# Kernel optimization log

Measured on AMD Instinct MI355X. Metric: run time of the kernel, lower is better.

The kernel has to match this reference:

```python
import jax, jax.numpy as jnp
import numpy as np

N_NODES = 50000
N_EDGES = 640000
N_REL = 8
IN_DIM = 128
HID_DIM = 128
OUT_DIM = 64


def setup_inputs() -> dict:
    key = jax.random.key(0)
    ks = jax.random.split(key, 8)
    features = jax.random.normal(ks[0], (N_NODES, IN_DIM), dtype=jnp.float32)
    src = jax.random.randint(ks[1], (N_EDGES,), 0, N_NODES, dtype=jnp.int32)
    dst = jax.random.randint(ks[2], (N_EDGES,), 0, N_NODES, dtype=jnp.int32)
    edge_types = jax.random.randint(ks[3], (N_EDGES,), 0, N_REL, dtype=jnp.int32)
    s1 = 1.0 / np.sqrt(IN_DIM)
    s2 = 1.0 / np.sqrt(HID_DIM)
    W1 = jax.random.normal(ks[4], (N_REL, IN_DIM, HID_DIM), dtype=jnp.float32) * s1
    W1_self = jax.random.normal(ks[5], (IN_DIM, HID_DIM), dtype=jnp.float32) * s1
    b1 = jnp.zeros((HID_DIM,), dtype=jnp.float32)
    W2 = jax.random.normal(ks[6], (N_REL, HID_DIM, OUT_DIM), dtype=jnp.float32) * s2
    W2_self = jax.random.normal(ks[7], (HID_DIM, OUT_DIM), dtype=jnp.float32) * s2
    b2 = jnp.zeros((OUT_DIM,), dtype=jnp.float32)
    return {"features": features, "src": src, "dst": dst, "edge_types": edge_types,
            "W1": W1, "W1_self": W1_self, "b1": b1,
            "W2": W2, "W2_self": W2_self, "b2": b2}


def _rel_graph_conv(h, src, dst, edge_types, W, W_self, b):
    # Precompute relation-specific transforms for all nodes: [R, N, Dout]
    rel = jnp.einsum('nd,rdo->rno', h, W)
    # Gather per-edge message W[etype(e)] @ h[src(e)]: [E, Dout]
    msg = rel[edge_types, src]
    # Scatter-sum to destination nodes
    agg = jax.ops.segment_sum(msg, dst, num_segments=h.shape[0])
    # Self-loop + bias (DGL RelGraphConv defaults: self_loop=True, bias=True)
    return agg + h @ W_self + b


def reference(features, src, dst, edge_types, W1, W1_self, b1, W2, W2_self, b2):
    h = jax.nn.relu(_rel_graph_conv(features, src, dst, edge_types, W1, W1_self, b1))
    logits = _rel_graph_conv(h, src, dst, edge_types, W2, W2_self, b2)
    return logits
```

## Files before the change

### kernel.cpp

```cpp
#include <hip/hip_runtime.h>
#include <hip/hip_bf16.h>
#include <stdint.h>

#define NN 50000
#define NE 640000
#define NR 8
#define NK (NR * NN)
#define NB2 ((NK + 1023) / 1024)

typedef short bf16x8 __attribute__((ext_vector_type(8)));
typedef float f32x4  __attribute__((ext_vector_type(4)));

__device__ __forceinline__ unsigned short f2bf(float f) {
    union { float f; unsigned u; } v; v.f = f;
    unsigned r = v.u + 0x7FFF + ((v.u >> 16) & 1);
    return (unsigned short)(r >> 16);
}

__global__ __launch_bounds__(256) void prep_all(
        const int* __restrict__ dst, const int* __restrict__ et, int* __restrict__ counts,
        const float* __restrict__ X, unsigned short* __restrict__ Xbf,
        const float* __restrict__ W1, const float* __restrict__ W1s, unsigned short* __restrict__ W1T,
        const float* __restrict__ W2, const float* __restrict__ W2s, unsigned short* __restrict__ W2T) {
    int b = blockIdx.x, t = threadIdx.x;
    if (b < 2500) {
        int e = b * 256 + t;
        atomicAdd(&counts[et[e] * NN + dst[e]], 1);
    } else if (b < 5625) {
        int i = (b - 2500) * 256 + t;
        const float4* pp = (const float4*)X + (size_t)i * 2;
        float4 a = pp[0], c = pp[1];
        uint4 o;
        o.x = (unsigned)f2bf(a.x) | ((unsigned)f2bf(a.y) << 16);
        o.y = (unsigned)f2bf(a.z) | ((unsigned)f2bf(a.w) << 16);
        o.z = (unsigned)f2bf(c.x) | ((unsigned)f2bf(c.y) << 16);
        o.w = (unsigned)f2bf(c.z) | ((unsigned)f2bf(c.w) << 16);
        ((uint4*)Xbf)[i] = o;
    } else if (b < 6201) {
        int idx = (b - 5625) * 256 + t;
        int k = idx & 127, c = idx >> 7;
        int r = c >> 7, o = c & 127;
        float v = (r < 8) ? W1[((size_t)r * 128 + k) * 128 + o]
                          : W1s[(size_t)k * 128 + o];
        W1T[idx] = f2bf(v);
    } else {
        int idx = (b - 6201) * 256 + t;
        int k = idx & 127, c = idx >> 7;
        int r = c / 64, o = c - r * 64;
        float v = (r < 8) ? W2[((size_t)r * 128 + k) * 64 + o]
                          : W2s[(size_t)k * 64 + o];
        W2T[idx] = f2bf(v);
    }
}

__global__ __launch_bounds__(1024) void blocksum_kernel(const int* __restrict__ counts,
                                                        int* __restrict__ bsum, int n) {
    __shared__ int ws[16];
    int i = blockIdx.x * 1024 + threadIdx.x;
    int v = (i < n) ? counts[i] : 0;
    #pragma unroll
    for (int d = 32; d > 0; d >>= 1) v += __shfl_down(v, d, 64);
    int wid = threadIdx.x >> 6, lane = threadIdx.x & 63;
    if (lane == 0) ws[wid] = v;
    __syncthreads();
    if (threadIdx.x < 16) {
        int s = ws[threadIdx.x];
        #pragma unroll
        for (int d = 8; d > 0; d >>= 1) s += __shfl_down(s, d, 16);
        if (threadIdx.x == 0) bsum[blockIdx.x] = s;
    }
}

__global__ __launch_bounds__(512) void scanbase_kernel(const int* __restrict__ bsum,
                                                       int* __restrict__ base,
                                                       int* __restrict__ total, int nb) {
    __shared__ int ws[8];
    int t = threadIdx.x, lane = t & 63, wid = t >> 6;
    int v = (t < nb) ? bsum[t] : 0;
    int incl = v;
    #pragma unroll
    for (int d = 1; d < 64; d <<= 1) {
        int nv = __shfl_up(incl, d, 64);
        if (lane >= d) incl += nv;
    }
    if (lane == 63) ws[wid] = incl;
    __syncthreads();
    if (t < 8) {
        int s = ws[t], si = s;
        #pragma unroll
        for (int d = 1; d < 8; d <<= 1) {
            int nv = __shfl_up(si, d, 64);
            if (t >= d) si += nv;
        }
        ws[t] = si - s;
    }
    __syncthreads();
    int excl = ws[wid] + incl - v;
    if (t < nb) base[t] = excl;
    if (t == 511) total[0] = ws[7] + incl;
}

__global__ __launch_bounds__(1024) void scanlocal_kernel(const int* __restrict__ counts,
                                                         const int* __restrict__ base,
                                                         int* __restrict__ offsets,
                                                         int* __restrict__ cursor, int n) {
    __shared__ int ws[16];
    __shared__ int wbase[16];
    int t = threadIdx.x;
    int i = blockIdx.x * 1024 + t;
    int v = (i < n) ? counts[i] : 0;
    int lane = t & 63, wid = t >> 6;
    int incl = v;
    #pragma unroll
    for (int d = 1; d < 64; d <<= 1) {
        int nv = __shfl_up(incl, d, 64);
        if (lane >= d) incl += nv;
    }
    if (lane == 63) ws[wid] = incl;
    __syncthreads();
    if (t < 16) {
        int s = ws[t], si = s;
        #pragma unroll
        for (int d = 1; d < 16; d <<= 1) {
            int nv = __shfl_up(si, d, 16);
            if (t >= d) si += nv;
        }
        wbase[t] = si - s;
    }
    __syncthreads();
    if (i < n) {
        int excl = base[blockIdx.x] + wbase[wid] + incl - v;
        offsets[i] = excl;
        cursor[i]  = excl;
    }
}

__global__ void fill2_kernel(const int* __restrict__ src, const int* __restrict__ dst,
                             const int* __restrict__ et, int* __restrict__ cursor,
                             int* __restrict__ esrc) {
    int e = blockIdx.x * 256 + threadIdx.x;
    if (e < NE) {
        int pos = atomicAdd(&cursor[et[e] * NN + dst[e]], 1);
        esrc[pos] = src[e];
    }
}

template<int NOUT, bool RELU, bool OUTBF16>
__global__ __launch_bounds__(256) void fused_layer(
        const unsigned short* __restrict__ A,
        const unsigned short* __restrict__ WT,
        const float* __restrict__ bias,
        const int* __restrict__ off2,
        const int* __restrict__ esrc,
        void* __restrict__ outp, int M) {
    constexpr int CW = NOUT / 4;
    constexpr int NJ = CW / 16;
    __shared__ unsigned short Asw[64 * 128];

    const int t = threadIdx.x;
    const int n0 = blockIdx.x * 64;
    const int bm = (M - n0 < 64) ? (M - n0) : 64;
    const int lane = t & 63;
    const int w = t >> 6;
    const int r15 = lane & 15;
    const int q = lane >> 4;

    const int key = t >> 2;
    const int sub = t & 3;
    const int kk = n0 + key;
    const bool kv = (kk < M);

    f32x4 acc[4][NJ] = {};

    auto do_mfma = [&](int rr) {
        #pragma unroll
        for (int ks = 0; ks < 4; ks++) {
            int c = (ks * 4 + q) ^ r15;
            bf16x8 af[4];
            #pragma unroll
            for (int i = 0; i < 4; i++)
                af[i] = *(const bf16x8*)((const char*)Asw + (i * 16 + r15) * 256 + (c << 4));
            #pragma unroll
            for (int j = 0; j < NJ; j++) {
                bf16x8 bf = *(const bf16x8*)(WT +
                    ((size_t)(rr * NOUT + w * CW + j * 16 + r15) << 7) + ks * 32 + q * 8);
                #pragma unroll
                for (int i = 0; i < 4; i++)
                    acc[i][j] = __builtin_amdgcn_mfma_f32_16x16x32_bf16(af[i], bf, acc[i][j], 0, 0, 0);
            }
        }
    };

    int e0 = kv ? off2[kk] : 0;
    int e1 = kv ? off2[kk + 1] : 0;

    #pragma unroll
    for (int kc = 0; kc < 4; kc++) {
        int g = t + kc * 256;
        int row = g >> 4, c = g & 15;
        uint4 v = make_uint4(0, 0, 0, 0);
        if (row < bm) v = *(const uint4*)(A + ((size_t)(n0 + row) << 7) + c * 8);
        *(uint4*)((char*)Asw + row * 256 + ((c ^ (row & 15)) << 4)) = v;
    }
    __syncthreads();
    do_mfma(8);

    for (int r = 0; r < 8; r++) {
        int e0n = 0, e1n = 0;
        if (r < 7 && kv) {
            e0n = off2[(r + 1) * NN + kk];
            e1n = off2[(r + 1) * NN + kk + 1];
        }

        float a[32];
        #pragma unroll
        for (int i = 0; i < 32; i++) a[i] = 0.f;

        const unsigned* base = (const unsigned*)A;
        for (int e = e0; e < e1; e += 4) {
            int rem = e1 - e;
            int i1 = (rem > 1) ? 1 : 0, i2 = (rem > 2) ? 2 : 0, i3 = (rem > 3) ? 3 : 0;
            int ss[4];
            ss[0] = esrc[e];
            ss[1] = esrc[e + i1];
            ss[2] = esrc[e + i2];
            ss[3] = esrc[e + i3];
            float wts[4];
            wts[0] = 1.f;
            wts[1] = i1 ? 1.f : 0.f;
            wts[2] = i2 ? 1.f : 0.f;
            wts[3] = i3 ? 1.f : 0.f;
            uint4 va[4][4];
            #pragma unroll
            for (int i = 0; i < 4; i++) {
                const uint4* rp = (const uint4*)(base + ((size_t)ss[i] << 6) + sub * 16);
                #pragma unroll
                for (int u = 0; u < 4; u++) va[i][u] = rp[u];
            }
            #pragma unroll
            for (int i = 0; i < 4; i++) {
                #pragma unroll
                for (int u = 0; u < 4; u++) {
                    unsigned uu[4] = {va[i][u].x, va[i][u].y, va[i][u].z, va[i][u].w};
                    #pragma unroll
                    for (int j = 0; j < 4; j++) {
                        a[u * 8 + j * 2 + 0] = fmaf(wts[i], __uint_as_float(uu[j] << 16), a[u * 8 + j * 2 + 0]);
                        a[u * 8 + j * 2 + 1] = fmaf(wts[i], __uint_as_float(uu[j] & 0xffff0000u), a[u * 8 + j * 2 + 1]);
                    }
                }
            }
        }
        __syncthreads();

        #pragma unroll
        for (int c4 = 0; c4 < 4; ++c4) {
            uint4 pv;
            pv.x = (unsigned)f2bf(a[c4 * 8 + 0]) | ((unsigned)f2bf(a[c4 * 8 + 1]) << 16);
            pv.y = (unsigned)f2bf(a[c4 * 8 + 2]) | ((unsigned)f2bf(a[c4 * 8 + 3]) << 16);
            pv.z = (unsigned)f2bf(a[c4 * 8 + 4]) | ((unsigned)f2bf(a[c4 * 8 + 5]) << 16);
            pv.w = (unsigned)f2bf(a[c4 * 8 + 6]) | ((unsigned)f2bf(a[c4 * 8 + 7]) << 16);
            int c = sub * 4 + c4;
            *(uint4*)((char*)Asw + key * 256 + ((c ^ (key & 15)) << 4)) = pv;
        }
        __syncthreads();

        do_mfma(r);
        e0 = e0n; e1 = e1n;
    }

    #pragma unroll
    for (int j = 0; j < NJ; j++) {
        int col = w * CW + j * 16 + r15;
        float bv = bias[col];
        #pragma unroll
        for (int i = 0; i < 4; i++) {
            #pragma unroll
            for (int reg = 0; reg < 4; reg++) {
                int m = n0 + i * 16 + q * 4 + reg;
                if (m < M) {
                    float v = acc[i][j][reg] + bv;
                    if (RELU) v = fmaxf(v, 0.f);
                    if (OUTBF16)
                        ((unsigned short*)outp)[(size_t)m * NOUT + col] = f2bf(v);
                    else
                        ((float*)outp)[(size_t)m * NOUT + col] = v;
                }
            }
        }
    }
}

extern "C" void kernel_launch(void* const* d_in, const int* in_sizes, int n_in,
                              void* d_out, int out_size, void* d_ws, size_t ws_size,
                              hipStream_t stream) {
    const float* X   = (const float*)d_in[0];
    const int*   src = (const int*)d_in[1];
    const int*   dst = (const int*)d_in[2];
    const int*   et  = (const int*)d_in[3];
    const float* W1  = (const float*)d_in[4];
    const float* W1s = (const float*)d_in[5];
    const float* b1  = (const float*)d_in[6];
    const float* W2  = (const float*)d_in[7];
    const float* W2s = (const float*)d_in[8];
    const float* b2  = (const float*)d_in[9];
    float* out = (float*)d_out;

    char* p = (char*)d_ws;
    unsigned short* Xbf = (unsigned short*)p; p += (size_t)NN * 128 * 2;
    unsigned short* hbf = (unsigned short*)p; p += (size_t)NN * 128 * 2;
    unsigned short* W1T = (unsigned short*)p; p += (size_t)9 * 128 * 128 * 2;
    unsigned short* W2T = (unsigned short*)p; p += (size_t)9 * 64 * 128 * 2;
    int* counts2 = (int*)p; p += (size_t)NK * 4;
    int* off2    = (int*)p; p += (size_t)(NK + 4) * 4;
    int* cursor2 = (int*)p; p += (size_t)NK * 4;
    int* esrc    = (int*)p; p += (size_t)NE * 4;
    int* bsum    = (int*)p; p += 512 * 4;
    int* bbase   = (int*)p; p += 512 * 4;

    hipMemsetAsync(counts2, 0, (size_t)NK * sizeof(int), stream);
    prep_all<<<6489, 256, 0, stream>>>(dst, et, counts2, X, Xbf,
                                       W1, W1s, W1T, W2, W2s, W2T);

    blocksum_kernel<<<NB2, 1024, 0, stream>>>(counts2, bsum, NK);
    scanbase_kernel<<<1, 512, 0, stream>>>(bsum, bbase, &off2[NK], NB2);
    scanlocal_kernel<<<NB2, 1024, 0, stream>>>(counts2, bbase, off2, cursor2, NK);
    fill2_kernel<<<(NE + 255) / 256, 256, 0, stream>>>(src, dst, et, cursor2, esrc);

    const int nblk = (NN + 63) / 64;

    fused_layer<128, true, true><<<nblk, 256, 0, stream>>>(
        Xbf, W1T, b1, off2, esrc, hbf, NN);
    fused_layer<64, false, false><<<nblk, 256, 0, stream>>>(
        hbf, W2T, b2, off2, esrc, out, NN);
}
```

Measured before the change: 327.9 us.

## Process two relations per iteration with double LDS buffers in fused layer

```diff
diff --git a/kernel.cpp b/kernel.cpp
--- a/kernel.cpp
+++ b/kernel.cpp
@@ -155,7 +155,7 @@
         void* __restrict__ outp, int M) {
     constexpr int CW = NOUT / 4;
     constexpr int NJ = CW / 16;
-    __shared__ unsigned short Asw[64 * 128];
+    __shared__ unsigned short Asw[2][64 * 128];
 
     const int t = threadIdx.x;
     const int n0 = blockIdx.x * 64;
@@ -172,14 +172,14 @@
 
     f32x4 acc[4][NJ] = {};
 
-    auto do_mfma = [&](int rr) {
+    auto do_mfma = [&](int b, int rr) {
         #pragma unroll
         for (int ks = 0; ks < 4; ks++) {
             int c = (ks * 4 + q) ^ r15;
             bf16x8 af[4];
             #pragma unroll
             for (int i = 0; i < 4; i++)
-                af[i] = *(const bf16x8*)((const char*)Asw + (i * 16 + r15) * 256 + (c << 4));
+                af[i] = *(const bf16x8*)((const char*)Asw[b] + (i * 16 + r15) * 256 + (c << 4));
             #pragma unroll
             for (int j = 0; j < NJ; j++) {
                 bf16x8 bf = *(const bf16x8*)(WT +
@@ -191,8 +191,24 @@
         }
     };
 
-    int e0 = kv ? off2[kk] : 0;
-    int e1 = kv ? off2[kk + 1] : 0;
+    auto accum32 = [&](float* a, const uint4* v, float wt) {
+        #pragma unroll
+        for (int u = 0; u < 4; u++) {
+            unsigned uu[4] = {v[u].x, v[u].y, v[u].z, v[u].w};
+            #pragma unroll
+            for (int j = 0; j < 4; j++) {
+                a[u * 8 + j * 2 + 0] = fmaf(wt, __uint_as_float(uu[j] << 16), a[u * 8 + j * 2 + 0]);
+                a[u * 8 + j * 2 + 1] = fmaf(wt, __uint_as_float(uu[j] & 0xffff0000u), a[u * 8 + j * 2 + 1]);
+            }
+        }
+    };
+
+    const unsigned* base = (const unsigned*)A;
+
+    int eA0 = kv ? off2[kk] : 0;
+    int eA1 = kv ? off2[kk + 1] : 0;
+    int eB0 = kv ? off2[NN + kk] : 0;
+    int eB1 = kv ? off2[NN + kk + 1] : 0;
 
     #pragma unroll
     for (int kc = 0; kc < 4; kc++) {
@@ -200,72 +216,98 @@
         int row = g >> 4, c = g & 15;
         uint4 v = make_uint4(0, 0, 0, 0);
         if (row < bm) v = *(const uint4*)(A + ((size_t)(n0 + row) << 7) + c * 8);
-        *(uint4*)((char*)Asw + row * 256 + ((c ^ (row & 15)) << 4)) = v;
-    }
-    __syncthreads();
-    do_mfma(8);
-
-    for (int r = 0; r < 8; r++) {
-        int e0n = 0, e1n = 0;
-        if (r < 7 && kv) {
-            e0n = off2[(r + 1) * NN + kk];
-            e1n = off2[(r + 1) * NN + kk + 1];
-        }
-
-        float a[32];
-        #pragma unroll
-        for (int i = 0; i < 32; i++) a[i] = 0.f;
-
-        const unsigned* base = (const unsigned*)A;
-        for (int e = e0; e < e1; e += 4) {
-            int rem = e1 - e;
-            int i1 = (rem > 1) ? 1 : 0, i2 = (rem > 2) ? 2 : 0, i3 = (rem > 3) ? 3 : 0;
-            int ss[4];
-            ss[0] = esrc[e];
-            ss[1] = esrc[e + i1];
-            ss[2] = esrc[e + i2];
-            ss[3] = esrc[e + i3];
-            float wts[4];
-            wts[0] = 1.f;
-            wts[1] = i1 ? 1.f : 0.f;
-            wts[2] = i2 ? 1.f : 0.f;
-            wts[3] = i3 ? 1.f : 0.f;
-            uint4 va[4][4];
-            #pragma unroll
-            for (int i = 0; i < 4; i++) {
-                const uint4* rp = (const uint4*)(base + ((size_t)ss[i] << 6) + sub * 16);
-                #pragma unroll
-                for (int u = 0; u < 4; u++) va[i][u] = rp[u];
-            }
-            #pragma unroll
-            for (int i = 0; i < 4; i++) {
-                #pragma unroll
-                for (int u = 0; u < 4; u++) {
-                    unsigned uu[4] = {va[i][u].x, va[i][u].y, va[i][u].z, va[i][u].w};
-                    #pragma unroll
-                    for (int j = 0; j < 4; j++) {
-                        a[u * 8 + j * 2 + 0] = fmaf(wts[i], __uint_as_float(uu[j] << 16), a[u * 8 + j * 2 + 0]);
-                        a[u * 8 + j * 2 + 1] = fmaf(wts[i], __uint_as_float(uu[j] & 0xffff0000u), a[u * 8 + j * 2 + 1]);
-                    }
-                }
-            }
+        *(uint4*)((char*)Asw[0] + row * 256 + ((c ^ (row & 15)) << 4)) = v;
+    }
+    __syncthreads();
+    do_mfma(0, 8);
+
+    #pragma unroll 1
+    for (int p = 0; p < 4; p++) {
+        const int rA = 2 * p, rB = 2 * p + 1;
+        int nA0 = 0, nA1 = 0, nB0 = 0, nB1 = 0;
+        if (p < 3 && kv) {
+            nA0 = off2[(rA + 2) * NN + kk];
+            nA1 = off2[(rA + 2) * NN + kk + 1];
+            nB0 = off2[(rB + 2) * NN + kk];
+            nB1 = off2[(rB + 2) * NN + kk + 1];
+        }
+
+        float a0[32], a1[32];
+        #pragma unroll
+        for (int i = 0; i < 32; i++) { a0[i] = 0.f; a1[i] = 0.f; }
+
+        int eA = eA0, eB = eB0;
+        while (eA < eA1 && eB < eB1) {
+            int av = (eA + 1 < eA1) ? 1 : 0;
+            int bv = (eB + 1 < eB1) ? 1 : 0;
+            int sA0 = esrc[eA], sA1 = esrc[eA + av];
+            int sB0 = esrc[eB], sB1 = esrc[eB + bv];
+            const uint4* pA0 = (const uint4*)(base + ((size_t)sA0 << 6) + sub * 16);
+            const uint4* pA1 = (const uint4*)(base + ((size_t)sA1 << 6) + sub * 16);
+            const uint4* pB0 = (const uint4*)(base + ((size_t)sB0 << 6) + sub * 16);
+            const uint4* pB1 = (const uint4*)(base + ((size_t)sB1 << 6) + sub * 16);
+            uint4 vA0[4], vA1[4], vB0[4], vB1[4];
+            #pragma unroll
+            for (int u = 0; u < 4; u++) vA0[u] = pA0[u];
+            #pragma unroll
+            for (int u = 0; u < 4; u++) vA1[u] = pA1[u];
+            #pragma unroll
+            for (int u = 0; u < 4; u++) vB0[u] = pB0[u];
+            #pragma unroll
+            for (int u = 0; u < 4; u++) vB1[u] = pB1[u];
+            accum32(a0, vA0, 1.f); accum32(a0, vA1, av ? 1.f : 0.f);
+            accum32(a1, vB0, 1.f); accum32(a1, vB1, bv ? 1.f : 0.f);
+            eA += 2; eB += 2;
+        }
+        while (eA < eA1) {
+            int av = (eA + 1 < eA1) ? 1 : 0;
+            int sA0 = esrc[eA], sA1 = esrc[eA + av];
+            const uint4* pA0 = (const uint4*)(base + ((size_t)sA0 << 6) + sub * 16);
+            const uint4* pA1 = (const uint4*)(base + ((size_t)sA1 << 6) + sub * 16);
+            uint4 vA0[4], vA1[4];
+            #pragma unroll
+            for (int u = 0; u < 4; u++) vA0[u] = pA0[u];
+            #pragma unroll
+            for (int u = 0; u < 4; u++) vA1[u] = pA1[u];
+            accum32(a0, vA0, 1.f); accum32(a0, vA1, av ? 1.f : 0.f);
+            eA += 2;
+        }
+        while (eB < eB1) {
+            int bv = (eB + 1 < eB1) ? 1 : 0;
+            int sB0 = esrc[eB], sB1 = esrc[eB + bv];
+            const uint4* pB0 = (const uint4*)(base + ((size_t)sB0 << 6) + sub * 16);
+            const uint4* pB1 = (const uint4*)(base + ((size_t)sB1 << 6) + sub * 16);
+            uint4 vB0[4], vB1[4];
+            #pragma unroll
+            for (int u = 0; u < 4; u++) vB0[u] = pB0[u];
+            #pragma unroll
+            for (int u = 0; u < 4; u++) vB1[u] = pB1[u];
+            accum32(a1, vB0, 1.f); accum32(a1, vB1, bv ? 1.f : 0.f);
+            eB += 2;
         }
         __syncthreads();
 
         #pragma unroll
         for (int c4 = 0; c4 < 4; ++c4) {
-            uint4 pv;
-            pv.x = (unsigned)f2bf(a[c4 * 8 + 0]) | ((unsigned)f2bf(a[c4 * 8 + 1]) << 16);
-            pv.y = (unsigned)f2bf(a[c4 * 8 + 2]) | ((unsigned)f2bf(a[c4 * 8 + 3]) << 16);
-            pv.z = (unsigned)f2bf(a[c4 * 8 + 4]) | ((unsigned)f2bf(a[c4 * 8 + 5]) << 16);
-            pv.w = (unsigned)f2bf(a[c4 * 8 + 6]) | ((unsigned)f2bf(a[c4 * 8 + 7]) << 16);
             int c = sub * 4 + c4;
-            *(uint4*)((char*)Asw + key * 256 + ((c ^ (key & 15)) << 4)) = pv;
+            int off = key * 256 + ((c ^ (key & 15)) << 4);
+            uint4 p0, p1;
+            p0.x = (unsigned)f2bf(a0[c4 * 8 + 0]) | ((unsigned)f2bf(a0[c4 * 8 + 1]) << 16);
+            p0.y = (unsigned)f2bf(a0[c4 * 8 + 2]) | ((unsigned)f2bf(a0[c4 * 8 + 3]) << 16);
+            p0.z = (unsigned)f2bf(a0[c4 * 8 + 4]) | ((unsigned)f2bf(a0[c4 * 8 + 5]) << 16);
+            p0.w = (unsigned)f2bf(a0[c4 * 8 + 6]) | ((unsigned)f2bf(a0[c4 * 8 + 7]) << 16);
+            p1.x = (unsigned)f2bf(a1[c4 * 8 + 0]) | ((unsigned)f2bf(a1[c4 * 8 + 1]) << 16);
+            p1.y = (unsigned)f2bf(a1[c4 * 8 + 2]) | ((unsigned)f2bf(a1[c4 * 8 + 3]) << 16);
+            p1.z = (unsigned)f2bf(a1[c4 * 8 + 4]) | ((unsigned)f2bf(a1[c4 * 8 + 5]) << 16);
+            p1.w = (unsigned)f2bf(a1[c4 * 8 + 6]) | ((unsigned)f2bf(a1[c4 * 8 + 7]) << 16);
+            *(uint4*)((char*)Asw[0] + off) = p0;
+            *(uint4*)((char*)Asw[1] + off) = p1;
         }
         __syncthreads();
 
-        do_mfma(r);
-        e0 = e0n; e1 = e1n;
+        do_mfma(0, rA);
+        do_mfma(1, rB);
+        eA0 = nA0; eA1 = nA1; eB0 = nB0; eB1 = nB1;
     }
 
     #pragma unroll
@@ -313,7 +355,7 @@
     int* counts2 = (int*)p; p += (size_t)NK * 4;
     int* off2    = (int*)p; p += (size_t)(NK + 4) * 4;
     int* cursor2 = (int*)p; p += (size_t)NK * 4;
-    int* esrc    = (int*)p; p += (size_t)NE * 4;
+    int* esrc    = (int*)p; p += (size_t)(NE + 16) * 4;
     int* bsum    = (int*)p; p += 512 * 4;
     int* bbase   = (int*)p; p += 512 * 4;
 
```

Measured after the change: 335.0 us. 2.2% more time.
